# Kernel optimization log

Hardware: AMD Instinct MI355X
Metric: run time of the kernel (lower is better)

Reference implementation:

```python
import jax, jax.numpy as jnp
import numpy as np

EPSILON = 1e-5
CUT_LO, CUT_HI = 0.0, 5.0


def _exp_normal_smear(dist, num_rbf):
    # dist: (..., 1) broadcast against num_rbf means -> (..., num_rbf)
    start = float(np.exp(-CUT_HI + CUT_LO))
    means = jnp.linspace(start, 1.0, num_rbf, dtype=dist.dtype)
    betas = jnp.full((num_rbf,), (2.0 / num_rbf * (1.0 - start)) ** -2, dtype=dist.dtype)
    alpha = 5.0 / (CUT_HI - CUT_LO)
    cutoff = 0.5 * (jnp.cos(np.pi * dist / CUT_HI) + 1.0) * (dist < CUT_HI)
    return cutoff * jnp.exp(-betas * (jnp.exp(alpha * (-dist + CUT_LO)) - means) ** 2)


def setup_inputs() -> dict:
    key = jax.random.key(0)
    k1, k2, k3, _ = jax.random.split(key, 4)
    B, N, K, H, O = 4, 16, 16, 64, 1
    x = jax.random.normal(k1, (B, N, 3), dtype=jnp.float32) * 3.0  # atom coords
    W = jax.random.normal(k2, (N, N, N, N, K, H), dtype=jnp.float32) * 0.02
    w_fc = jax.random.normal(k3, (H, O), dtype=jnp.float32) * 0.1
    b_fc = jnp.zeros((O,), dtype=jnp.float32)
    return {"x": x, "W": W, "w_fc": w_fc, "b_fc": b_fc}


def reference(x, W, w_fc, b_fc):
    # x: (B, N, 3); W: (N, N, N, N, K, H)
    K = W.shape[-2]
    diff = x[..., :, None, :] - x[..., None, :, :]          # (B, N, N, 3)
    norm_sq = jnp.sum(diff * diff, axis=-1, keepdims=True) + EPSILON  # (B, N, N, 1)
    norm = jnp.sqrt(norm_sq)
    diff = diff / norm_sq                                     # note: divide by norm^2 (faithful)
    smear = _exp_normal_smear(norm, K)                        # (B, N, N, K)
    basis = smear[..., None] * diff[..., None, :]             # (B, N, N, K, 3)
    h = jnp.einsum('zabkc,zdekc,abdeko->zao', basis, basis, W)  # (B, N, H)
    return jax.nn.silu(h) @ w_fc + b_fc                       # (B, N, O)
```

## Files before the change

### kernel.cpp

```cpp
#include <hip/hip_runtime.h>
#include <math.h>


#define NJ 65536
#define BPA 128

typedef float f32x4 __attribute__((ext_vector_type(4)));

static constexpr double D_START = 0.006737946999085467;

#define ACC8(pA, pB, wA, wB) do {                                              \
    acc[0][0] += pA.x * wA.x + pB.x * wB.x; acc[0][1] += pA.x * wA.y + pB.x * wB.y; \
    acc[0][2] += pA.x * wA.z + pB.x * wB.z; acc[0][3] += pA.x * wA.w + pB.x * wB.w; \
    acc[1][0] += pA.y * wA.x + pB.y * wB.x; acc[1][1] += pA.y * wA.y + pB.y * wB.y; \
    acc[1][2] += pA.y * wA.z + pB.y * wB.z; acc[1][3] += pA.y * wA.w + pB.y * wB.w; \
    acc[2][0] += pA.z * wA.x + pB.z * wB.x; acc[2][1] += pA.z * wA.y + pB.z * wB.y; \
    acc[2][2] += pA.z * wA.z + pB.z * wB.z; acc[2][3] += pA.z * wA.w + pB.z * wB.w; \
    acc[3][0] += pA.w * wA.x + pB.w * wB.x; acc[3][1] += pA.w * wA.y + pB.w * wB.y; \
    acc[3][2] += pA.w * wA.z + pB.w * wB.z; acc[3][3] += pA.w * wA.w + pB.w * wB.w; \
} while (0)

__device__ __forceinline__ bool pair_basis(const float* __restrict__ x,
                                           int z, int p, int q, int k,
                                           float& bx, float& by, float& bz) {
    const float* xp = x + (z * 16 + p) * 3;
    const float* xq = x + (z * 16 + q) * 3;
    float d0 = xp[0] - xq[0], d1 = xp[1] - xq[1], d2 = xp[2] - xq[2];
    float nsq = d0 * d0 + d1 * d1 + d2 * d2 + 1e-5f;
    float nrm = sqrtf(nsq);
    if (nrm >= 5.0f) return false;
    float cut = 0.5f * (cosf(nrm * 0.6283185307179586f) + 1.0f);
    float ex = expf(-nrm);
    const float START = (float)D_START;
    const float STEP  = (float)((1.0 - D_START) / 15.0);
    const float BETA  = (float)(1.0 / ((0.125 * (1.0 - D_START)) * (0.125 * (1.0 - D_START))));
    float m = START + STEP * (float)k;
    float dmm = ex - m;
    float s = cut * expf(-BETA * dmm * dmm) / nsq;
    bx = s * d0; by = s * d1; bz = s * d2;
    return true;
}

__global__ __launch_bounds__(256) void k_main(const f32x4* __restrict__ W4,
                                              const float* __restrict__ x,
                                              float* __restrict__ part) {
    int a   = blockIdx.x >> 7;
    int blk = blockIdx.x & (BPA - 1);

    __shared__ f32x4 p_lds[512];
    __shared__ float red[4][256];

    int t = threadIdx.x;
    f32x4 p0 = {0.f, 0.f, 0.f, 0.f}, p1 = {0.f, 0.f, 0.f, 0.f};
    {
        int e = t >> 4, k = t & 15;
        int b = blk >> 3, dd = (blk & 7) * 2;
        #pragma unroll
        for (int z = 0; z < 4; ++z) {
            float ux, uy, uz;
            if (pair_basis(x, z, a, b, k, ux, uy, uz)) {
                float vx, vy, vz;
                if (pair_basis(x, z, dd, e, k, vx, vy, vz))
                    p0[z] = ux * vx + uy * vy + uz * vz;
                if (pair_basis(x, z, dd + 1, e, k, vx, vy, vz))
                    p1[z] = ux * vx + uy * vy + uz * vz;
            }
        }
    }
    bool f0 = (fabsf(p0.x) + fabsf(p0.y) + fabsf(p0.z) + fabsf(p0.w)) != 0.0f;
    bool f1 = (fabsf(p1.x) + fabsf(p1.y) + fabsf(p1.z) + fabsf(p1.w)) != 0.0f;
    unsigned long long bal0 = __ballot(f0);
    unsigned long long bal1 = __ballot(f1);
    p_lds[t]       = p0;
    p_lds[t + 256] = p1;
    __syncthreads();

    int wave = t >> 6;
    int lane = t & 63;
    int og   = lane & 15;
    int rsub = lane >> 4;

    unsigned mask = 0;
    #pragma unroll
    for (int g = 0; g < 8; ++g) {
        if ((bal0 >> (8 * g)) & 0xFFull) mask |= 1u << g;
        if ((bal1 >> (8 * g)) & 0xFFull) mask |= 1u << (g + 8);
    }

    float acc[4][4] = {{0.f, 0.f, 0.f, 0.f}, {0.f, 0.f, 0.f, 0.f},
                       {0.f, 0.f, 0.f, 0.f}, {0.f, 0.f, 0.f, 0.f}};
    size_t rowbase = (size_t)a * NJ + (size_t)blk * 512;
    while (mask) {
        int g1 = __builtin_ctz(mask);
        mask &= mask - 1;
        int rloc1 = ((g1 & 8) ? 256 : 0) + wave * 64 + (g1 & 7) * 8 + rsub;
        f32x4 pA1 = p_lds[rloc1];
        f32x4 pB1 = p_lds[rloc1 + 4];
        f32x4 wA1 = W4[(rowbase + rloc1) * 16 + og];
        f32x4 wB1 = W4[(rowbase + rloc1 + 4) * 16 + og];
        if (mask) {
            int g2 = __builtin_ctz(mask);
            mask &= mask - 1;
            int rloc2 = ((g2 & 8) ? 256 : 0) + wave * 64 + (g2 & 7) * 8 + rsub;
            f32x4 pA2 = p_lds[rloc2];
            f32x4 pB2 = p_lds[rloc2 + 4];
            f32x4 wA2 = W4[(rowbase + rloc2) * 16 + og];
            f32x4 wB2 = W4[(rowbase + rloc2 + 4) * 16 + og];
            ACC8(pA1, pB1, wA1, wB1);
            ACC8(pA2, pB2, wA2, wB2);
        } else {
            ACC8(pA1, pB1, wA1, wB1);
        }
    }

    #pragma unroll
    for (int z = 0; z < 4; ++z) {
        #pragma unroll
        for (int c = 0; c < 4; ++c) {
            float v = acc[z][c];
            v += __shfl_xor(v, 16);
            v += __shfl_xor(v, 32);
            acc[z][c] = v;
        }
    }
    if (rsub == 0) {
        #pragma unroll
        for (int z = 0; z < 4; ++z) {
            #pragma unroll
            for (int c = 0; c < 4; ++c)
                red[wave][z * 64 + og * 4 + c] = acc[z][c];
        }
    }
    __syncthreads();
    float s = red[0][t] + red[1][t] + red[2][t] + red[3][t];
    part[((size_t)a * BPA + blk) * 256 + t] = s;
}

__global__ void k_out(const float* __restrict__ part, const float* __restrict__ w_fc,
                      const float* __restrict__ b_fc, float* __restrict__ out) {
    int z = blockIdx.x >> 4, a = blockIdx.x & 15;
    int o = threadIdx.x & 63, bq = threadIdx.x >> 6;
    float s = 0.f;
    for (int blk = bq; blk < BPA; blk += 4)
        s += part[((size_t)a * BPA + blk) * 256 + z * 64 + o];
    __shared__ float red[4][64];
    red[bq][o] = s;
    __syncthreads();
    if (threadIdx.x < 64) {
        float h = red[0][o] + red[1][o] + red[2][o] + red[3][o];
        float v = h * (1.0f / (1.0f + expf(-h))) * w_fc[o];
        #pragma unroll
        for (int off = 32; off >= 1; off >>= 1) v += __shfl_xor(v, off);
        if (o == 0) out[z * 16 + a] = v + b_fc[0];
    }
}

extern "C" void kernel_launch(void* const* d_in, const int* in_sizes, int n_in,
                              void* d_out, int out_size, void* d_ws, size_t ws_size,
                              hipStream_t stream) {
    const float* x    = (const float*)d_in[0];
    const float* W    = (const float*)d_in[1];
    const float* w_fc = (const float*)d_in[2];
    const float* b_fc = (const float*)d_in[3];
    float* ws  = (float*)d_ws;
    float* out = (float*)d_out;

    float* part = ws;

    k_main<<<16 * BPA, 256, 0, stream>>>((const f32x4*)W, x, part);
    k_out<<<64, 256, 0, stream>>>(part, w_fc, b_fc, out);
}
```

Before: 28.20 us.

## Share pair geometry via LDS and balance sparse row groups across waves

Per-pair distance, cutoff and exponential terms are now computed once by 132 threads into shared memory instead of redundantly by every thread for every basis index k. The nonzero-row masks of all waves are combined in shared memory, and active row groups are handed out round-robin to the four waves so the sparse W streaming is balanced. The main loop is restructured to issue the next group's loads before accumulating the previous one. The cost is an extra barrier and shared-memory traffic, plus coarser 16-row group granularity in the mask, which may load some all-zero rows.

```diff
diff --git a/kernel.cpp b/kernel.cpp
--- a/kernel.cpp
+++ b/kernel.cpp
@@ -6,6 +6,7 @@
 #define BPA 128
 
 typedef float f32x4 __attribute__((ext_vector_type(4)));
+typedef unsigned int u32;
 
 static constexpr double D_START = 0.006737946999085467;
 
@@ -20,52 +21,63 @@
     acc[3][2] += pA.w * wA.z + pB.w * wB.z; acc[3][3] += pA.w * wA.w + pB.w * wB.w; \
 } while (0)
 
-__device__ __forceinline__ bool pair_basis(const float* __restrict__ x,
-                                           int z, int p, int q, int k,
-                                           float& bx, float& by, float& bz) {
-    const float* xp = x + (z * 16 + p) * 3;
-    const float* xq = x + (z * 16 + q) * 3;
-    float d0 = xp[0] - xq[0], d1 = xp[1] - xq[1], d2 = xp[2] - xq[2];
-    float nsq = d0 * d0 + d1 * d1 + d2 * d2 + 1e-5f;
-    float nrm = sqrtf(nsq);
-    if (nrm >= 5.0f) return false;
-    float cut = 0.5f * (cosf(nrm * 0.6283185307179586f) + 1.0f);
-    float ex = expf(-nrm);
-    const float START = (float)D_START;
-    const float STEP  = (float)((1.0 - D_START) / 15.0);
-    const float BETA  = (float)(1.0 / ((0.125 * (1.0 - D_START)) * (0.125 * (1.0 - D_START))));
-    float m = START + STEP * (float)k;
-    float dmm = ex - m;
-    float s = cut * expf(-BETA * dmm * dmm) / nsq;
-    bx = s * d0; by = s * d1; bz = s * d2;
-    return true;
-}
-
 __global__ __launch_bounds__(256) void k_main(const f32x4* __restrict__ W4,
                                               const float* __restrict__ x,
                                               float* __restrict__ part) {
     int a   = blockIdx.x >> 7;
     int blk = blockIdx.x & (BPA - 1);
+    int b  = blk >> 3, dd = (blk & 7) * 2;
 
     __shared__ f32x4 p_lds[512];
     __shared__ float red[4][256];
+    __shared__ float s_d0[132], s_d1[132], s_d2[132], s_cc[132], s_ex[132];
+    __shared__ u32 s_gm[4];
+
+    const float START = (float)D_START;
+    const float STEP  = (float)((1.0 - D_START) / 15.0);
+    const float BETA  = (float)(1.0 / ((0.125 * (1.0 - D_START)) * (0.125 * (1.0 - D_START))));
 
     int t = threadIdx.x;
-    f32x4 p0 = {0.f, 0.f, 0.f, 0.f}, p1 = {0.f, 0.f, 0.f, 0.f};
-    {
-        int e = t >> 4, k = t & 15;
-        int b = blk >> 3, dd = (blk & 7) * 2;
-        #pragma unroll
-        for (int z = 0; z < 4; ++z) {
-            float ux, uy, uz;
-            if (pair_basis(x, z, a, b, k, ux, uy, uz)) {
-                float vx, vy, vz;
-                if (pair_basis(x, z, dd, e, k, vx, vy, vz))
-                    p0[z] = ux * vx + uy * vy + uz * vz;
-                if (pair_basis(x, z, dd + 1, e, k, vx, vy, vz))
-                    p1[z] = ux * vx + uy * vy + uz * vz;
-            }
+
+    if (t < 132) {
+        int z = t / 33, pr = t - z * 33;
+        int p, q;
+        if (pr == 0)      { p = a;      q = b; }
+        else if (pr < 17) { p = dd;     q = pr - 1; }
+        else              { p = dd + 1; q = pr - 17; }
+        const float* xp = x + (z * 16 + p) * 3;
+        const float* xq = x + (z * 16 + q) * 3;
+        float d0 = xp[0] - xq[0], d1 = xp[1] - xq[1], d2 = xp[2] - xq[2];
+        float nsq = d0 * d0 + d1 * d1 + d2 * d2 + 1e-5f;
+        float nrm = sqrtf(nsq);
+        float cc = 0.f, ex = 0.f;
+        if (nrm < 5.0f) {
+            cc = 0.5f * (cosf(nrm * 0.6283185307179586f) + 1.0f) / nsq;
+            ex = expf(-nrm);
         }
+        s_d0[t] = d0; s_d1[t] = d1; s_d2[t] = d2; s_cc[t] = cc; s_ex[t] = ex;
+    }
+    __syncthreads();
+
+    int e = t >> 4, k = t & 15;
+    float mk = START + STEP * (float)k;
+    f32x4 p0, p1;
+    #pragma unroll
+    for (int z = 0; z < 4; ++z) {
+        int base = z * 33;
+        float exu = s_ex[base];
+        float su  = s_cc[base] * expf(-BETA * (exu - mk) * (exu - mk));
+        float du0 = s_d0[base], du1 = s_d1[base], du2 = s_d2[base];
+        int i0 = base + 1 + e;
+        float exv0 = s_ex[i0];
+        float sv0  = s_cc[i0] * expf(-BETA * (exv0 - mk) * (exv0 - mk));
+        float dot0 = du0 * s_d0[i0] + du1 * s_d1[i0] + du2 * s_d2[i0];
+        p0[z] = su * sv0 * dot0;
+        int i1 = base + 17 + e;
+        float exv1 = s_ex[i1];
+        float sv1  = s_cc[i1] * expf(-BETA * (exv1 - mk) * (exv1 - mk));
+        float dot1 = du0 * s_d0[i1] + du1 * s_d1[i1] + du2 * s_d2[i1];
+        p1[z] = su * sv1 * dot1;
     }
     bool f0 = (fabsf(p0.x) + fabsf(p0.y) + fabsf(p0.z) + fabsf(p0.w)) != 0.0f;
     bool f1 = (fabsf(p1.x) + fabsf(p1.y) + fabsf(p1.z) + fabsf(p1.w)) != 0.0f;
@@ -73,44 +85,48 @@
     unsigned long long bal1 = __ballot(f1);
     p_lds[t]       = p0;
     p_lds[t + 256] = p1;
-    __syncthreads();
 
     int wave = t >> 6;
     int lane = t & 63;
     int og   = lane & 15;
     int rsub = lane >> 4;
 
-    unsigned mask = 0;
+    u32 m0 = 0, m1 = 0;
     #pragma unroll
-    for (int g = 0; g < 8; ++g) {
-        if ((bal0 >> (8 * g)) & 0xFFull) mask |= 1u << g;
-        if ((bal1 >> (8 * g)) & 0xFFull) mask |= 1u << (g + 8);
+    for (int i = 0; i < 4; ++i) {
+        if ((bal0 >> (16 * i)) & 0xFFFFull) m0 |= 3u << (2 * i);
+        if ((bal1 >> (16 * i)) & 0xFFFFull) m1 |= 3u << (2 * i);
+    }
+    if (lane == 0) s_gm[wave] = m0 | (m1 << 8);
+    __syncthreads();
+    unsigned long long m64 = 0;
+    #pragma unroll
+    for (int i = 0; i < 4; ++i) {
+        u32 v = s_gm[i];
+        m64 |= (unsigned long long)(v & 0xFFu) << (8 * i);
+        m64 |= (unsigned long long)((v >> 8) & 0xFFu) << (32 + 8 * i);
     }
 
     float acc[4][4] = {{0.f, 0.f, 0.f, 0.f}, {0.f, 0.f, 0.f, 0.f},
                        {0.f, 0.f, 0.f, 0.f}, {0.f, 0.f, 0.f, 0.f}};
     size_t rowbase = (size_t)a * NJ + (size_t)blk * 512;
-    while (mask) {
-        int g1 = __builtin_ctz(mask);
-        mask &= mask - 1;
-        int rloc1 = ((g1 & 8) ? 256 : 0) + wave * 64 + (g1 & 7) * 8 + rsub;
-        f32x4 pA1 = p_lds[rloc1];
-        f32x4 pB1 = p_lds[rloc1 + 4];
-        f32x4 wA1 = W4[(rowbase + rloc1) * 16 + og];
-        f32x4 wB1 = W4[(rowbase + rloc1 + 4) * 16 + og];
-        if (mask) {
-            int g2 = __builtin_ctz(mask);
-            mask &= mask - 1;
-            int rloc2 = ((g2 & 8) ? 256 : 0) + wave * 64 + (g2 & 7) * 8 + rsub;
-            f32x4 pA2 = p_lds[rloc2];
-            f32x4 pB2 = p_lds[rloc2 + 4];
-            f32x4 wA2 = W4[(rowbase + rloc2) * 16 + og];
-            f32x4 wB2 = W4[(rowbase + rloc2 + 4) * 16 + og];
-            ACC8(pA1, pB1, wA1, wB1);
-            ACC8(pA2, pB2, wA2, wB2);
-        } else {
-            ACC8(pA1, pB1, wA1, wB1);
+    {
+        int idx = 0;
+        bool have = false;
+        f32x4 pAp, pBp, wAp, wBp;
+        while (m64) {
+            int g = __builtin_ctzll(m64);
+            m64 &= m64 - 1;
+            if ((idx++ & 3) != wave) continue;
+            int rloc = g * 8 + rsub;
+            f32x4 pA = p_lds[rloc];
+            f32x4 pB = p_lds[rloc + 4];
+            f32x4 wA = W4[(rowbase + rloc) * 16 + og];
+            f32x4 wB = W4[(rowbase + rloc + 4) * 16 + og];
+            if (have) ACC8(pAp, pBp, wAp, wBp);
+            pAp = pA; pBp = pB; wAp = wA; wBp = wB; have = true;
         }
+        if (have) ACC8(pAp, pBp, wAp, wBp);
     }
 
     #pragma unroll
```

Measured after the change: 28.73 us. Within noise of the previous version (+1.9%).

## Fuse final reduction into main kernel via fixed-point atomics and last-block ticket

Applied to the files above, without the earlier changes.

Drops the separate k_out kernel and its partial-sum buffer. Each block converts its partial sums to 64-bit fixed-point and atomically adds them into a per-atom accumulator. A per-atom ticket counter lets the last finishing block apply SiLU, the output projection and the bias. This saves a kernel launch and the partial-sum round trip, but adds a memset launch, global atomic contention, and quantisation error from the fixed-point scaling.

```diff
diff --git a/kernel.cpp b/kernel.cpp
--- a/kernel.cpp
+++ b/kernel.cpp
@@ -4,8 +4,11 @@
 
 #define NJ 65536
 #define BPA 128
+#define FPSCALE 268435456.0f
 
 typedef float f32x4 __attribute__((ext_vector_type(4)));
+typedef unsigned int u32;
+typedef unsigned long long u64;
 
 static constexpr double D_START = 0.006737946999085467;
 
@@ -43,12 +46,17 @@
 
 __global__ __launch_bounds__(256) void k_main(const f32x4* __restrict__ W4,
                                               const float* __restrict__ x,
-                                              float* __restrict__ part) {
+                                              const float* __restrict__ w_fc,
+                                              const float* __restrict__ b_fc,
+                                              u64* __restrict__ hacc,
+                                              u32* __restrict__ done,
+                                              float* __restrict__ out) {
     int a   = blockIdx.x >> 7;
     int blk = blockIdx.x & (BPA - 1);
 
     __shared__ f32x4 p_lds[512];
     __shared__ float red[4][256];
+    __shared__ u32 s_ticket;
 
     int t = threadIdx.x;
     f32x4 p0 = {0.f, 0.f, 0.f, 0.f}, p1 = {0.f, 0.f, 0.f, 0.f};
@@ -133,26 +141,21 @@
     }
     __syncthreads();
     float s = red[0][t] + red[1][t] + red[2][t] + red[3][t];
-    part[((size_t)a * BPA + blk) * 256 + t] = s;
-}
 
-__global__ void k_out(const float* __restrict__ part, const float* __restrict__ w_fc,
-                      const float* __restrict__ b_fc, float* __restrict__ out) {
-    int z = blockIdx.x >> 4, a = blockIdx.x & 15;
-    int o = threadIdx.x & 63, bq = threadIdx.x >> 6;
-    float s = 0.f;
-    for (int blk = bq; blk < BPA; blk += 4)
-        s += part[((size_t)a * BPA + blk) * 256 + z * 64 + o];
-    __shared__ float red[4][64];
-    red[bq][o] = s;
+    long long q = (long long)llrintf(s * FPSCALE);
+    atomicAdd(&hacc[a * 256 + t], (u64)q);
     __syncthreads();
-    if (threadIdx.x < 64) {
-        float h = red[0][o] + red[1][o] + red[2][o] + red[3][o];
-        float v = h * (1.0f / (1.0f + expf(-h))) * w_fc[o];
-        #pragma unroll
-        for (int off = 32; off >= 1; off >>= 1) v += __shfl_xor(v, off);
-        if (o == 0) out[z * 16 + a] = v + b_fc[0];
-    }
+    if (t == 0) s_ticket = atomicAdd(&done[a], 1u);
+    __syncthreads();
+    if (s_ticket != BPA - 1) return;
+
+    u64 raw = atomicAdd(&hacc[a * 256 + t], 0ULL);
+    float h = (float)(long long)raw * (1.0f / FPSCALE);
+    int o = t & 63;
+    float v = h * (1.0f / (1.0f + expf(-h))) * w_fc[o];
+    #pragma unroll
+    for (int off = 32; off >= 1; off >>= 1) v += __shfl_xor(v, off);
+    if (o == 0) out[wave * 16 + a] = v + b_fc[0];
 }
 
 extern "C" void kernel_launch(void* const* d_in, const int* in_sizes, int n_in,
@@ -162,11 +165,12 @@
     const float* W    = (const float*)d_in[1];
     const float* w_fc = (const float*)d_in[2];
     const float* b_fc = (const float*)d_in[3];
-    float* ws  = (float*)d_ws;
     float* out = (float*)d_out;
 
-    float* part = ws;
+    u64* hacc = (u64*)d_ws;
+    u32* done = (u32*)((char*)d_ws + 32768);
 
-    k_main<<<16 * BPA, 256, 0, stream>>>((const f32x4*)W, x, part);
-    k_out<<<64, 256, 0, stream>>>(part, w_fc, b_fc, out);
+    (void)hipMemsetAsync(d_ws, 0, 32768 + 64, stream);
+    k_main<<<16 * BPA, 256, 0, stream>>>((const f32x4*)W, x, w_fc, b_fc,
+                                         hacc, done, out);
 }
```

Result: slower. 39.27 us (+39.2%).
